# Kernel optimization log

Measured on AMD Instinct MI355X. Metric: run time of the kernel, lower is better.

## Reference

```python
import jax, jax.numpy as jnp
import numpy as np

N_WAY, N_SHOT, N_SEG = 3, 1, 4
SEGLEN, C, H, W = 16, 3, 112, 112
REG, COST_ALPHA, PHI = 7.0, 0.4, 1.0
SINK_ITERS = 100
# eval-mode BatchNorm with fresh stats (mean=0, var=1, gamma=1, beta=0) -> pure scale
BN_SCALE = np.float32(1.0 / np.sqrt(1.0 + 1e-5))

PARAM_NAMES = ['conv1_w', 'conv1_b', 'conv2_w', 'conv2_b', 'conv3a_w', 'conv3a_b',
               'conv3b_w', 'conv3b_b', 'conv4a_w', 'conv4a_b', 'conv4b_w', 'conv4b_b',
               'conv5a_w', 'conv5a_b', 'conv5b_w', 'conv5b_b', 'fc6_w', 'fc6_b',
               'fc7_w', 'fc7_b']


def _conv3d(x, w, b):
    y = jax.lax.conv_general_dilated(x, w, (1, 1, 1), [(1, 1)] * 3,
                                     dimension_numbers=('NCDHW', 'OIDHW', 'NCDHW'))
    return y + b[None, :, None, None, None]


def _maxpool(x, k, s, p=(0, 0, 0)):
    return jax.lax.reduce_window(x, -jnp.inf, jax.lax.max,
                                 (1, 1) + k, (1, 1) + s,
                                 [(0, 0), (0, 0)] + [(q, q) for q in p])


def _encode(x, p):
    r = jax.nn.relu
    x = r(BN_SCALE * _conv3d(x, p['conv1_w'], p['conv1_b']))
    x = _maxpool(x, (1, 2, 2), (1, 2, 2))
    x = r(BN_SCALE * _conv3d(x, p['conv2_w'], p['conv2_b']))
    x = _maxpool(x, (2, 2, 2), (2, 2, 2))
    x = r(_conv3d(x, p['conv3a_w'], p['conv3a_b']))
    x = r(BN_SCALE * _conv3d(x, p['conv3b_w'], p['conv3b_b']))
    x = _maxpool(x, (2, 2, 2), (2, 2, 2))
    x = r(_conv3d(x, p['conv4a_w'], p['conv4a_b']))
    x = r(BN_SCALE * _conv3d(x, p['conv4b_w'], p['conv4b_b']))
    x = _maxpool(x, (2, 2, 2), (2, 2, 2))
    x = r(_conv3d(x, p['conv5a_w'], p['conv5a_b']))
    x = r(BN_SCALE * _conv3d(x, p['conv5b_w'], p['conv5b_b']))
    x = _maxpool(x, (2, 2, 2), (2, 2, 2), (0, 1, 1))  # -> (N, 512, 1, 4, 4)
    x = x.reshape(-1, 8192)
    x = r(BN_SCALE * (x @ p['fc6_w'].T + p['fc6_b']))  # dropout identity in eval
    x = r(BN_SCALE * (x @ p['fc7_w'].T + p['fc7_b']))
    return x


def _positional_cost():
    t = jnp.arange(N_SEG, dtype=jnp.float32) / N_SEG
    d2 = (t[:, None] - t[None, :]) ** 2
    return jnp.exp(-(1.0 / PHI ** 2) * (1.0 / (d2 + 1.0)))


def _sinkhorn(cost):  # cost: (Q, S, n, n), uniform marginals 1/n
    n = cost.shape[-1]
    a = jnp.full((n,), 1.0 / n, cost.dtype)
    K = jnp.exp(-REG * cost)
    u0 = jnp.full(cost.shape[:-1], 1.0 / n, cost.dtype)

    def body(u, _):
        v = a / (jnp.einsum('qsij,qsi->qsj', K, u) + 1e-9)
        u = a / (jnp.einsum('qsij,qsj->qsi', K, v) + 1e-9)
        return u, None

    u, _ = jax.lax.scan(body, u0, None, length=SINK_ITERS)
    v = a / (jnp.einsum('qsij,qsi->qsj', K, u) + 1e-9)
    return u[..., :, None] * K * v[..., None, :]


def _forward(support_set, query_set, p):
    ts, tq = support_set.shape[0], query_set.shape[0]
    # (N, n_seg, seglen, c, h, w) -> (N*n_seg, c, seglen, h, w)
    sp = jnp.swapaxes(support_set, 2, 3).reshape(-1, C, SEGLEN, H, W)
    qr = jnp.swapaxes(query_set, 2, 3).reshape(-1, C, SEGLEN, H, W)
    sp = _encode(sp, p).reshape(ts, N_SEG, -1)
    qr = _encode(qr, p).reshape(tq, N_SEG, -1)
    qn = qr / (jnp.linalg.norm(qr, axis=-1, keepdims=True) + 1e-8)
    sn = sp / (jnp.linalg.norm(sp, axis=-1, keepdims=True) + 1e-8)
    sem_cost = 1.0 - jnp.einsum('qid,sjd->qsij', qn, sn)  # (Q, S, n_seg, n_seg)
    # positional cost only regularizes the OT solve; transport cost uses sem_cost
    solve_cost = sem_cost + COST_ALPHA * _positional_cost()
    plan = _sinkhorn(solve_cost)
    trans_cost = jnp.sum(plan * sem_cost, axis=(-2, -1))
    trans_cost = trans_cost.reshape(tq, N_WAY, N_SHOT).mean(-1)
    return -trans_cost


def setup_inputs() -> dict:
    key = jax.random.key(0)
    ks = iter(jax.random.split(key, 24))

    def cw(o, i):
        return jax.random.normal(next(ks), (o, i, 3, 3, 3), jnp.float32) * np.float32(np.sqrt(2.0 / (i * 27)))

    def fw(o, i):
        return jax.random.normal(next(ks), (o, i), jnp.float32) * np.float32(np.sqrt(2.0 / i))

    z = lambda n: jnp.zeros((n,), jnp.float32)
    return dict(
        support_set=jax.random.normal(next(ks), (N_WAY * N_SHOT, N_SEG, SEGLEN, C, H, W), jnp.float32),
        query_set=jax.random.normal(next(ks), (N_WAY, N_SEG, SEGLEN, C, H, W), jnp.float32),
        conv1_w=cw(64, 3), conv1_b=z(64),
        conv2_w=cw(128, 64), conv2_b=z(128),
        conv3a_w=cw(256, 128), conv3a_b=z(256),
        conv3b_w=cw(256, 256), conv3b_b=z(256),
        conv4a_w=cw(512, 256), conv4a_b=z(512),
        conv4b_w=cw(512, 512), conv4b_b=z(512),
        conv5a_w=cw(512, 512), conv5a_b=z(512),
        conv5b_w=cw(512, 512), conv5b_b=z(512),
        fc6_w=fw(4096, 8192), fc6_b=z(4096),
        fc7_w=fw(4096, 4096), fc7_b=z(4096),
    )


def reference(support_set, query_set, conv1_w, conv1_b, conv2_w, conv2_b,
              conv3a_w, conv3a_b, conv3b_w, conv3b_b, conv4a_w, conv4a_b,
              conv4b_w, conv4b_b, conv5a_w, conv5a_b, conv5b_w, conv5b_b,
              fc6_w, fc6_b, fc7_w, fc7_b):
    p = dict(zip(PARAM_NAMES, (conv1_w, conv1_b, conv2_w, conv2_b, conv3a_w, conv3a_b,
                               conv3b_w, conv3b_b, conv4a_w, conv4a_b, conv4b_w, conv4b_b,
                               conv5a_w, conv5a_b, conv5b_w, conv5b_b, fc6_w, fc6_b,
                               fc7_w, fc7_b)))
    return _forward(support_set, query_set, p)
```

## Files before the change

kernel.cpp:

```cpp
#include <hip/hip_runtime.h>
#include <hip/hip_bf16.h>
#include <cmath>

#define BN_SCALE_F 0.9999950000374997f

typedef __attribute__((ext_vector_type(8))) short short8;
typedef __attribute__((ext_vector_type(4))) float floatx4;

static __device__ __forceinline__ ushort f2bf(float x) {
    union { float f; unsigned u; } c; c.f = x;
    unsigned r = (c.u + 0x7FFFu + ((c.u >> 16) & 1u)) >> 16;
    return (ushort)r;
}
static __device__ __forceinline__ float bf2f(ushort h) {
    union { unsigned u; float f; } c; c.u = ((unsigned)h) << 16;
    return c.f;
}

__global__ __launch_bounds__(256) void repack_kernel(
    const float* __restrict__ w, ushort* __restrict__ oh, ushort* __restrict__ ol,
    int CI, int total)
{
    int idx = blockIdx.x * 256 + threadIdx.x;
    if (idx >= total) return;
    int ci = idx % CI;
    int t  = (idx / CI) % 27;
    int co = idx / (CI * 27);
    float v = w[((size_t)co * CI + ci) * 27 + t];
    ushort h = f2bf(v);
    oh[idx] = h;
    ol[idx] = f2bf(v - bf2f(h));
}

__global__ __launch_bounds__(256) void conv1_ndhwc(
    const float* __restrict__ sup, const float* __restrict__ qry, int clipBase,
    const float* __restrict__ wgt, const float* __restrict__ bias,
    ushort* __restrict__ outH, ushort* __restrict__ outL)
{
    __shared__ float sIn[4][10][12];
    __shared__ float sW[16][28];
    const int tid = threadIdx.x;
    const int bw = blockIdx.x % 14;
    const int bh = (blockIdx.x / 14) % 14;
    const int bd = blockIdx.x / 196;
    const int coL = tid >> 4;
    const int co  = blockIdx.y * 16 + coL;
    const int sp  = tid & 15;
    const int sh = sp >> 2, sw = sp & 3;
    const int n = blockIdx.z;
    const int clip = clipBase + n;
    const float* src = (clip < 12) ? (sup + (size_t)clip * 602112)
                                   : (qry + (size_t)(clip - 12) * 602112);
    const int d0 = 2 * bd, h0 = 8 * bh, w0 = 8 * bw;

    float acc[8] = {0.f,0.f,0.f,0.f,0.f,0.f,0.f,0.f};
    for (int ci = 0; ci < 3; ci++) {
        for (int t = tid; t < 832; t += 256) {
            if (t < 400) {
                int pd = t / 100; int rem = t - pd * 100;
                int ph = rem / 10; int pw = rem - ph * 10;
                int gd = d0 - 1 + pd, gh = h0 - 1 + ph, gw = w0 - 1 + pw;
                float v = 0.f;
                if ((unsigned)gd < 16u && (unsigned)gh < 112u && (unsigned)gw < 112u)
                    v = src[(size_t)gd * 37632 + ci * 12544 + gh * 112 + gw];
                sIn[pd][ph][pw] = v;
            } else {
                int t2 = t - 400;
                if (t2 < 432) {
                    int cl = t2 / 27, k = t2 - cl * 27;
                    sW[cl][k] = wgt[((size_t)(blockIdx.y * 16 + cl) * 3 + ci) * 27 + k];
                }
            }
        }
        __syncthreads();
        float wr[27];
#pragma unroll
        for (int k = 0; k < 27; k++) wr[k] = sW[coL][k];
#pragma unroll
        for (int dd = 0; dd < 4; dd++) {
            float qv[16];
#pragma unroll
            for (int hh = 0; hh < 4; hh++)
#pragma unroll
                for (int ww = 0; ww < 4; ww++)
                    qv[hh * 4 + ww] = sIn[dd][2 * sh + hh][2 * sw + ww];
#pragma unroll
            for (int kd = 0; kd < 3; kd++) {
                int deltad = dd - kd;
                if (deltad < 0 || deltad > 1) continue;
#pragma unroll
                for (int kh = 0; kh < 3; kh++)
#pragma unroll
                    for (int kw = 0; kw < 3; kw++) {
                        float wv = wr[kd * 9 + kh * 3 + kw];
#pragma unroll
                        for (int dh = 0; dh < 2; dh++)
#pragma unroll
                            for (int dw = 0; dw < 2; dw++)
                                acc[deltad * 4 + dh * 2 + dw] =
                                    fmaf(wv, qv[(dh + kh) * 4 + (dw + kw)],
                                         acc[deltad * 4 + dh * 2 + dw]);
                    }
            }
        }
        __syncthreads();
    }
    const float b = __ldg(bias + co);
    const int oh = 4 * bh + sh, ow = 4 * bw + sw;
#pragma unroll
    for (int dd = 0; dd < 2; dd++) {
        float m = 0.f;
#pragma unroll
        for (int k = 0; k < 4; k++) m = fmaxf(m, (acc[dd * 4 + k] + b) * BN_SCALE_F);
        size_t idx = ((((size_t)n * 16 + (d0 + dd)) * 56 + oh) * 56 + ow) * 64 + co;
        ushort h = f2bf(m);
        outH[idx] = h;
        outL[idx] = f2bf(m - bf2f(h));
    }
}

template<int CIN,int COUT,int D,int H,int W,int MODE>
__global__ __launch_bounds__(256,1) void conv_mfma(
    const ushort* __restrict__ inH, const ushort* __restrict__ inL,
    const ushort* __restrict__ wH,  const ushort* __restrict__ wL,
    const float* __restrict__ bias,
    ushort* __restrict__ outH, ushort* __restrict__ outL, float* __restrict__ outF)
{
    constexpr int TW = (W + 7) / 8;
    constexpr int TH = (H + 7) / 8;
    __shared__ ushort sMem[19200 * 2 + 6144 * 2];
    ushort* sPH = sMem;
    ushort* sPL = sMem + 19200;
    ushort* sWH = sMem + 38400;
    ushort* sWL = sMem + 44544;

    const int tid = threadIdx.x;
    const int lane = tid & 63;
    const int wv = tid >> 6;
    const int n15 = lane & 15;
    const int g4 = lane >> 4;
    const int tw = blockIdx.x % TW;
    const int th = (blockIdx.x / TW) % TH;
    const int td = blockIdx.x / (TW * TH);
    const int coG0 = blockIdx.y * 64;
    const int n = blockIdx.z;

    int sdv[4], shv[4], swv[4];
#pragma unroll
    for (int spg = 0; spg < 4; spg++) {
        int s = wv * 64 + spg * 16 + n15;
        sdv[spg] = s >> 6; shv[spg] = (s >> 3) & 7; swv[spg] = s & 7;
    }

    const size_t inBase = (size_t)n * CIN * D * H * W;

    floatx4 acc[4][4];
#pragma unroll
    for (int i = 0; i < 4; i++)
#pragma unroll
        for (int j = 0; j < 4; j++) acc[i][j] = (floatx4){0.f, 0.f, 0.f, 0.f};

    uint4 pfH[3], pfL[3];

    for (int c0 = 0; c0 < CIN; c0 += 32) {
        for (int t = tid; t < 2400; t += 256) {
            int pos = t >> 2, g = t & 3;
            int pd = pos / 100; int rem = pos - pd * 100;
            int ph = rem / 10;  int pw = rem - ph * 10;
            int gd = td * 4 - 1 + pd;
            int gh = th * 8 - 1 + ph;
            int gw = tw * 8 - 1 + pw;
            uint4 vh = {0u,0u,0u,0u}, vl = {0u,0u,0u,0u};
            if ((unsigned)gd < (unsigned)D && (unsigned)gh < (unsigned)H && (unsigned)gw < (unsigned)W) {
                size_t gi = inBase + (((size_t)gd * H + gh) * W + gw) * CIN + c0 + g * 8;
                vh = *(const uint4*)(inH + gi);
                vl = *(const uint4*)(inL + gi);
            }
            *(uint4*)(sPH + pos * 32 + g * 8) = vh;
            *(uint4*)(sPL + pos * 32 + g * 8) = vl;
        }
        if (c0 == 0) {
#pragma unroll
            for (int k = 0; k < 3; k++) {
                int t = tid + k * 256;
                int kw = t >> 8, col = (t >> 2) & 63, g8 = t & 3;
                size_t src = ((size_t)(coG0 + col) * 27 + kw) * CIN + g8 * 8;
                pfH[k] = *(const uint4*)(wH + src);
                pfL[k] = *(const uint4*)(wL + src);
            }
        }
        __syncthreads();

        for (int row = 0; row < 9; row++) {
#pragma unroll
            for (int k = 0; k < 3; k++) {
                int t = tid + k * 256;
                int kw = t >> 8, col = (t >> 2) & 63, g8 = t & 3;
                int dst = (kw * 64 + col) * 32 + g8 * 8;
                *(uint4*)(sWH + dst) = pfH[k];
                *(uint4*)(sWL + dst) = pfL[k];
            }
            __syncthreads();
            {
                int nc0 = c0, nrow = row + 1;
                if (nrow == 9) { nrow = 0; nc0 = c0 + 32; }
                if (nc0 < CIN) {
#pragma unroll
                    for (int k = 0; k < 3; k++) {
                        int t = tid + k * 256;
                        int kw = t >> 8, col = (t >> 2) & 63, g8 = t & 3;
                        size_t src = ((size_t)(coG0 + col) * 27 + nrow * 3 + kw) * CIN + nc0 + g8 * 8;
                        pfH[k] = *(const uint4*)(wH + src);
                        pfL[k] = *(const uint4*)(wL + src);
                    }
                }
            }
            const int kd = row / 3, kh = row - kd * 3;
            int pbase[4];
#pragma unroll
            for (int spg = 0; spg < 4; spg++)
                pbase[spg] = ((sdv[spg] + kd) * 10 + shv[spg] + kh) * 10 + swv[spg];
#pragma unroll
            for (int kw = 0; kw < 3; kw++) {
                short8 Bh[4], Bl[4];
#pragma unroll
                for (int spg = 0; spg < 4; spg++) {
                    int off = (pbase[spg] + kw) * 32 + g4 * 8;
                    Bh[spg] = *(const short8*)(sPH + off);
                    Bl[spg] = *(const short8*)(sPL + off);
                }
#pragma unroll
                for (int cog = 0; cog < 4; cog++) {
                    int offA = (kw * 64 + cog * 16 + n15) * 32 + g4 * 8;
                    short8 Ah = *(const short8*)(sWH + offA);
                    short8 Al = *(const short8*)(sWL + offA);
#pragma unroll
                    for (int spg = 0; spg < 4; spg++) {
                        acc[cog][spg] = __builtin_amdgcn_mfma_f32_16x16x32_bf16(Ah, Bh[spg], acc[cog][spg], 0, 0, 0);
                        acc[cog][spg] = __builtin_amdgcn_mfma_f32_16x16x32_bf16(Ah, Bl[spg], acc[cog][spg], 0, 0, 0);
                        acc[cog][spg] = __builtin_amdgcn_mfma_f32_16x16x32_bf16(Al, Bh[spg], acc[cog][spg], 0, 0, 0);
                    }
                }
            }
            __syncthreads();
        }
    }

    float* sEp = (float*)sMem;
#pragma unroll
    for (int cog = 0; cog < 4; cog++)
#pragma unroll
        for (int spg = 0; spg < 4; spg++) {
            int sp = wv * 64 + spg * 16 + n15;
#pragma unroll
            for (int r = 0; r < 4; r++) {
                int co = cog * 16 + g4 * 4 + r;
                sEp[sp * 65 + co] = acc[cog][spg][r];
            }
        }
    __syncthreads();

    const int co = tid & 63;
    const int coG = coG0 + co;
    const float b = __ldg(bias + coG);

    if constexpr (MODE == 0) {
#pragma unroll 4
        for (int i = 0; i < 64; i++) {
            int sp = i * 4 + (tid >> 6);
            int ld = sp >> 6, lh = (sp >> 3) & 7, lw = sp & 7;
            int gd = td * 4 + ld, gh = th * 8 + lh, gw = tw * 8 + lw;
            if (gh < H && gw < W) {
                float y = fmaxf(sEp[sp * 65 + co] + b, 0.f);
                size_t idx = ((((size_t)n * D + gd) * H + gh) * W + gw) * COUT + coG;
                ushort h = f2bf(y);
                outH[idx] = h;
                outL[idx] = f2bf(y - bf2f(h));
            }
        }
    } else {
        constexpr int OD = D / 2, OH = H / 2, OW = W / 2;
#pragma unroll
        for (int i = 0; i < 8; i++) {
            int pp = i * 4 + (tid >> 6);
            int ppd = pp >> 4, pph = (pp >> 2) & 3, ppw = pp & 3;
            int gpd = td * 2 + ppd, gph = th * 4 + pph, gpw = tw * 4 + ppw;
            if (gph < OH && gpw < OW) {
                float m = -1e30f;
#pragma unroll
                for (int dd = 0; dd < 2; dd++)
#pragma unroll
                    for (int dh = 0; dh < 2; dh++)
#pragma unroll
                        for (int dw = 0; dw < 2; dw++) {
                            int sp = (ppd * 2 + dd) * 64 + (pph * 2 + dh) * 8 + (ppw * 2 + dw);
                            m = fmaxf(m, sEp[sp * 65 + co]);
                        }
                float y = fmaxf((m + b) * BN_SCALE_F, 0.f);
                if constexpr (MODE == 1) {
                    size_t idx = ((((size_t)n * OD + gpd) * OH + gph) * OW + gpw) * COUT + coG;
                    ushort h = f2bf(y);
                    outH[idx] = h;
                    outL[idx] = f2bf(y - bf2f(h));
                } else {
                    size_t idx = ((((size_t)n * COUT + coG) * OD + gpd) * OH + gph) * OW + gpw;
                    outF[idx] = y;
                }
            }
        }
    }
}

template<int CIN,int COUT,int D,int H,int W,int MODE>
__global__ __launch_bounds__(256) void conv_tile(
    const float* __restrict__ in,
    const float* __restrict__ wgt, const float* __restrict__ bias,
    float* __restrict__ out)
{
    constexpr int PAD = (MODE == 3) ? 1 : 0;
    constexpr int OD  = (MODE == 0) ? D : D / 2;
    constexpr int OH  = (MODE == 0) ? H : (H + 2 * PAD) / 2;
    constexpr int OW  = (MODE == 0) ? W : (W + 2 * PAD) / 2;
    constexpr int TH  = (MODE == 0) ? (H + 7) / 8 : (OH + 3) / 4;
    constexpr int TW  = (MODE == 0) ? (W + 7) / 8 : (OW + 3) / 4;
    constexpr int HW  = H * W;
    constexpr int CC  = 2;

    __shared__ float sIn[CC][4][10][12];
    __shared__ float sW[CC][16][28];

    const int tid = threadIdx.x;
    const int bw = blockIdx.x % TW;
    const int bh = (blockIdx.x / TW) % TH;
    const int bd = blockIdx.x / (TW * TH);
    const int coL = tid >> 4;
    const int co  = blockIdx.y * 16 + coL;
    const int sp  = tid & 15;
    const int sh = sp >> 2, sw = sp & 3;
    const int n = blockIdx.z;

    const int d0 = 2 * bd, h0 = 8 * bh - PAD, w0 = 8 * bw - PAD;
    const int ht = h0 + 2 * sh, wt = w0 + 2 * sw;

    const float* src = in + (size_t)n * CIN * D * HW;

    float acc[8] = {0.f,0.f,0.f,0.f,0.f,0.f,0.f,0.f};

    for (int ci0 = 0; ci0 < CIN; ci0 += CC) {
        for (int t = tid; t < CC * 400 + CC * 432; t += 256) {
            if (t < CC * 400) {
                int c = t / 400, r = t % 400;
                int pd = r / 100, ph = (r / 10) % 10, pw = r % 10;
                int gd = d0 - 1 + pd, gh = h0 - 1 + ph, gw = w0 - 1 + pw;
                float v = 0.f;
                if (gd >= 0 && gd < D && gh >= 0 && gh < H && gw >= 0 && gw < W)
                    v = src[(size_t)(ci0 + c) * D * HW + gd * HW + gh * W + gw];
                sIn[c][pd][ph][pw] = v;
            } else {
                int t2 = t - CC * 400;
                int c = t2 / 432, r = t2 % 432;
                int cl = r / 27, k = r % 27;
                sW[c][cl][k] = wgt[((size_t)(blockIdx.y * 16 + cl) * CIN + (ci0 + c)) * 27 + k];
            }
        }
        __syncthreads();
        for (int c = 0; c < CC; c++) {
            float wr[27];
#pragma unroll
            for (int k = 0; k < 27; k++) wr[k] = sW[c][coL][k];
#pragma unroll
            for (int dd = 0; dd < 4; dd++) {
                float qv[16];
#pragma unroll
                for (int hh = 0; hh < 4; hh++)
#pragma unroll
                    for (int ww = 0; ww < 4; ww++)
                        qv[hh * 4 + ww] = sIn[c][dd][2 * sh + hh][2 * sw + ww];
#pragma unroll
                for (int kd = 0; kd < 3; kd++) {
                    int deltad = dd - kd;
                    if (deltad < 0 || deltad > 1) continue;
#pragma unroll
                    for (int kh = 0; kh < 3; kh++)
#pragma unroll
                        for (int kw = 0; kw < 3; kw++) {
                            float wv = wr[kd * 9 + kh * 3 + kw];
#pragma unroll
                            for (int dh = 0; dh < 2; dh++)
#pragma unroll
                                for (int dw = 0; dw < 2; dw++)
                                    acc[deltad * 4 + dh * 2 + dw] =
                                        fmaf(wv, qv[(dh + kh) * 4 + (dw + kw)],
                                             acc[deltad * 4 + dh * 2 + dw]);
                        }
                }
            }
        }
        __syncthreads();
    }

    const float b = __ldg(bias + co);
    if constexpr (MODE == 0) {
#pragma unroll
        for (int dd = 0; dd < 2; dd++) {
            int d = d0 + dd; if (d >= D) continue;
#pragma unroll
            for (int dh = 0; dh < 2; dh++) {
                int h = ht + dh; if (h < 0 || h >= H) continue;
#pragma unroll
                for (int dw = 0; dw < 2; dw++) {
                    int w = wt + dw; if (w < 0 || w >= W) continue;
                    out[(((size_t)n * COUT + co) * D + d) * HW + h * W + w] =
                        fmaxf(acc[dd * 4 + dh * 2 + dw] + b, 0.f);
                }
            }
        }
    } else {
        int oh = 4 * bh + sh, ow = 4 * bw + sw;
        if (oh < OH && ow < OW) {
            float m = 0.f;
#pragma unroll
            for (int dd2 = 0; dd2 < 2; dd2++)
#pragma unroll
                for (int dh = 0; dh < 2; dh++) {
                    int h = ht + dh; if (PAD && (h < 0 || h >= H)) continue;
#pragma unroll
                    for (int dw = 0; dw < 2; dw++) {
                        int w = wt + dw; if (PAD && (w < 0 || w >= W)) continue;
                        m = fmaxf(m, (acc[dd2 * 4 + dh * 2 + dw] + b) * BN_SCALE_F);
                    }
                }
            out[(((size_t)n * COUT + co) * OD + bd) * (OH * OW) + oh * OW + ow] = m;
        }
    }
}

__global__ __launch_bounds__(256) void fc_kernel(
    const float* __restrict__ x, const float* __restrict__ wgt,
    const float* __restrict__ bias, float* __restrict__ out,
    int K, int Cout, int total)
{
    int gt = blockIdx.x * 256 + threadIdx.x;
    int wid = gt >> 6;
    int lane = gt & 63;
    if (wid >= total) return;
    int co = wid % Cout; int n = wid / Cout;
    const float4* xp = (const float4*)(x + (size_t)n * K);
    const float4* wp = (const float4*)(wgt + (size_t)co * K);
    int K4 = K >> 2;
    float s = 0.f;
    for (int k = lane; k < K4; k += 64) {
        float4 a = __ldg(xp + k), b = __ldg(wp + k);
        s += a.x * b.x + a.y * b.y + a.z * b.z + a.w * b.w;
    }
#pragma unroll
    for (int off = 32; off > 0; off >>= 1) s += __shfl_down(s, off, 64);
    if (lane == 0) {
        float y = (s + __ldg(bias + co)) * BN_SCALE_F;
        out[wid] = fmaxf(y, 0.f);
    }
}

__global__ __launch_bounds__(256) void dots_kernel(
    const float* __restrict__ feat, float* __restrict__ dots)
{
    int task = blockIdx.x; int tid = threadIdx.x;
    int ra, rb;
    if (task < 24) { ra = task; rb = task; }
    else {
        int t = task - 24;
        int q = t / 48; int r = t % 48;
        int i = r / 12; int s = (r % 12) / 4; int j = r % 4;
        ra = 12 + q * 4 + i;
        rb = s * 4 + j;
    }
    const float4* A = (const float4*)(feat + (size_t)ra * 4096);
    const float4* B = (const float4*)(feat + (size_t)rb * 4096);
    float acc = 0.f;
    for (int k = tid; k < 1024; k += 256) {
        float4 a = A[k], b = B[k];
        acc += a.x * b.x + a.y * b.y + a.z * b.z + a.w * b.w;
    }
#pragma unroll
    for (int off = 32; off > 0; off >>= 1) acc += __shfl_down(acc, off, 64);
    __shared__ float red[4];
    if ((tid & 63) == 0) red[tid >> 6] = acc;
    __syncthreads();
    if (tid == 0) dots[task] = red[0] + red[1] + red[2] + red[3];
}

__global__ __launch_bounds__(64) void sinkhorn_kernel(
    const float* __restrict__ dots, float* __restrict__ out)
{
    int t = threadIdx.x;
    if (t >= 9) return;
    int q = t / 3, s = t % 3;
    float Km[16], sem[16];
#pragma unroll
    for (int i = 0; i < 4; i++) {
        float nq = sqrtf(dots[12 + q * 4 + i]) + 1e-8f;
#pragma unroll
        for (int j = 0; j < 4; j++) {
            float ns = sqrtf(dots[s * 4 + j]) + 1e-8f;
            float d = dots[24 + q * 48 + i * 12 + s * 4 + j];
            float c = 1.0f - d / (nq * ns);
            float ti = i * 0.25f, tj = j * 0.25f;
            float d2 = (ti - tj) * (ti - tj);
            float pc = expf(-1.0f / (d2 + 1.0f));
            sem[i * 4 + j] = c;
            Km[i * 4 + j] = expf(-7.0f * (c + 0.4f * pc));
        }
    }
    float u[4] = {0.25f, 0.25f, 0.25f, 0.25f}, v[4];
    for (int it = 0; it < 100; it++) {
#pragma unroll
        for (int j = 0; j < 4; j++) {
            float sj = Km[j] * u[0] + Km[4 + j] * u[1] + Km[8 + j] * u[2] + Km[12 + j] * u[3];
            v[j] = 0.25f / (sj + 1e-9f);
        }
#pragma unroll
        for (int i = 0; i < 4; i++) {
            float si = Km[i * 4] * v[0] + Km[i * 4 + 1] * v[1] + Km[i * 4 + 2] * v[2] + Km[i * 4 + 3] * v[3];
            u[i] = 0.25f / (si + 1e-9f);
        }
    }
#pragma unroll
    for (int j = 0; j < 4; j++) {
        float sj = Km[j] * u[0] + Km[4 + j] * u[1] + Km[8 + j] * u[2] + Km[12 + j] * u[3];
        v[j] = 0.25f / (sj + 1e-9f);
    }
    float tc = 0.f;
#pragma unroll
    for (int i = 0; i < 4; i++)
#pragma unroll
        for (int j = 0; j < 4; j++)
            tc += u[i] * Km[i * 4 + j] * v[j] * sem[i * 4 + j];
    out[q * 3 + s] = -tc;
}

extern "C" void kernel_launch(void* const* d_in, const int* in_sizes, int n_in,
                              void* d_out, int out_size, void* d_ws, size_t ws_size,
                              hipStream_t stream)
{
    const float* sup = (const float*)d_in[0];
    const float* qry = (const float*)d_in[1];
    const float* w1  = (const float*)d_in[2];  const float* b1  = (const float*)d_in[3];
    const float* w2  = (const float*)d_in[4];  const float* b2  = (const float*)d_in[5];
    const float* w3a = (const float*)d_in[6];  const float* b3a = (const float*)d_in[7];
    const float* w3b = (const float*)d_in[8];  const float* b3b = (const float*)d_in[9];
    const float* w4a = (const float*)d_in[10]; const float* b4a = (const float*)d_in[11];
    const float* w4b = (const float*)d_in[12]; const float* b4b = (const float*)d_in[13];
    const float* w5a = (const float*)d_in[14]; const float* b5a = (const float*)d_in[15];
    const float* w5b = (const float*)d_in[16]; const float* b5b = (const float*)d_in[17];
    const float* w6  = (const float*)d_in[18]; const float* b6  = (const float*)d_in[19];
    const float* w7  = (const float*)d_in[20]; const float* b7  = (const float*)d_in[21];
    float* out = (float*)d_out;

    char* wsB = (char*)d_ws;
    size_t off = 0;
    auto carve = [&](size_t bytes) -> char* {
        char* p = wsB + off;
        off = (off + bytes + 255) & ~(size_t)255;
        return p;
    };

    const int RW2 = 128 * 27 * 64, RW3a = 256 * 27 * 128, RW3b = 256 * 27 * 256;
    const int RW4a = 512 * 27 * 256, RW4b = 512 * 27 * 512;
    ushort* w2H  = (ushort*)carve((size_t)RW2 * 2);  ushort* w2L  = (ushort*)carve((size_t)RW2 * 2);
    ushort* w3aH = (ushort*)carve((size_t)RW3a * 2); ushort* w3aL = (ushort*)carve((size_t)RW3a * 2);
    ushort* w3bH = (ushort*)carve((size_t)RW3b * 2); ushort* w3bL = (ushort*)carve((size_t)RW3b * 2);
    ushort* w4aH = (ushort*)carve((size_t)RW4a * 2); ushort* w4aL = (ushort*)carve((size_t)RW4a * 2);
    ushort* w4bH = (ushort*)carve((size_t)RW4b * 2); ushort* w4bL = (ushort*)carve((size_t)RW4b * 2);

    float* x4b24 = (float*)carve((size_t)24 * 50176 * 4);
    float* x5a24 = (float*)carve((size_t)24 * 50176 * 4);
    float* x5b24 = (float*)carve((size_t)24 * 8192 * 4);
    float* fc6o  = (float*)carve((size_t)24 * 4096 * 4);
    float* feat  = (float*)carve((size_t)24 * 4096 * 4);
    float* dotsb = (float*)carve(256 * 4);

    const size_t fixed = off;
    const long long P1 = 3211264LL, P2 = 802816LL;
    const long long perG = (P1 + P2) * 2 * 2;
    int G = 1;
    const int cands[8] = {24, 12, 8, 6, 4, 3, 2, 1};
    for (int k = 0; k < 8; k++) {
        if (fixed + (size_t)(perG * cands[k]) + 4096 <= ws_size) { G = cands[k]; break; }
    }
    ushort* AH = (ushort*)carve((size_t)G * P1 * 2);
    ushort* AL = (ushort*)carve((size_t)G * P1 * 2);
    ushort* BH = (ushort*)carve((size_t)G * P2 * 2);
    ushort* BL = (ushort*)carve((size_t)G * P2 * 2);

    repack_kernel<<<(RW2  + 255) / 256, 256, 0, stream>>>(w2,  w2H,  w2L,  64,  RW2);
    repack_kernel<<<(RW3a + 255) / 256, 256, 0, stream>>>(w3a, w3aH, w3aL, 128, RW3a);
    repack_kernel<<<(RW3b + 255) / 256, 256, 0, stream>>>(w3b, w3bH, w3bL, 256, RW3b);
    repack_kernel<<<(RW4a + 255) / 256, 256, 0, stream>>>(w4a, w4aH, w4aL, 256, RW4a);
    repack_kernel<<<(RW4b + 255) / 256, 256, 0, stream>>>(w4b, w4bH, w4bL, 512, RW4b);

    for (int base = 0; base < 24; base += G) {
        conv1_ndhwc<<<dim3(1568, 4, G), 256, 0, stream>>>(sup, qry, base, w1, b1, AH, AL);
        conv_mfma<64, 128, 16, 56, 56, 1><<<dim3(196, 2, G), 256, 0, stream>>>(
            AH, AL, w2H, w2L, b2, BH, BL, nullptr);
        conv_mfma<128, 256, 8, 28, 28, 0><<<dim3(32, 4, G), 256, 0, stream>>>(
            BH, BL, w3aH, w3aL, b3a, AH, AL, nullptr);
        conv_mfma<256, 256, 8, 28, 28, 1><<<dim3(32, 4, G), 256, 0, stream>>>(
            AH, AL, w3bH, w3bL, b3b, BH, BL, nullptr);
        conv_mfma<256, 512, 4, 14, 14, 0><<<dim3(4, 8, G), 256, 0, stream>>>(
            BH, BL, w4aH, w4aL, b4a, AH, AL, nullptr);
        conv_mfma<512, 512, 4, 14, 14, 2><<<dim3(4, 8, G), 256, 0, stream>>>(
            AH, AL, w4bH, w4bL, b4b, nullptr, nullptr, x4b24 + (size_t)base * 50176);
    }

    conv_tile<512, 512, 2, 7, 7, 0><<<dim3(1, 32, 24), 256, 0, stream>>>(x4b24, w5a, b5a, x5a24);
    conv_tile<512, 512, 2, 7, 7, 3><<<dim3(1, 32, 24), 256, 0, stream>>>(x5a24, w5b, b5b, x5b24);
    int t6 = 24 * 4096;
    fc_kernel<<<(t6 * 64 + 255) / 256, 256, 0, stream>>>(x5b24, w6, b6, fc6o, 8192, 4096, t6);
    fc_kernel<<<(t6 * 64 + 255) / 256, 256, 0, stream>>>(fc6o, w7, b7, feat, 4096, 4096, t6);
    dots_kernel<<<168, 256, 0, stream>>>(feat, dotsb);
    sinkhorn_kernel<<<1, 64, 0, stream>>>(dotsb, out);
}
```

Measured before the change: 10.78 ms.

## Move conv5 to MFMA path, swizzle LDS, batch FC over samples

Conv5a and conv5b now run on the split-bf16 MFMA conv kernel, with a new epilogue mode that fuses the padded max-pool and writes the flattened features. The scalar fp32 conv_tile kernel is removed. LDS tiles for inputs and weights get an XOR swizzle to reduce bank conflicts. The FC kernel now computes all 24 samples per weight row, so each weight is read once instead of 24 times, at the cost of 24 accumulators per lane and more registers.

```diff
diff --git a/kernel.cpp b/kernel.cpp
--- a/kernel.cpp
+++ b/kernel.cpp
@@ -176,8 +176,9 @@
                 vh = *(const uint4*)(inH + gi);
                 vl = *(const uint4*)(inL + gi);
             }
-            *(uint4*)(sPH + pos * 32 + g * 8) = vh;
-            *(uint4*)(sPL + pos * 32 + g * 8) = vl;
+            int sg = g ^ ((pos >> 1) & 3);
+            *(uint4*)(sPH + pos * 32 + sg * 8) = vh;
+            *(uint4*)(sPL + pos * 32 + sg * 8) = vl;
         }
         if (c0 == 0) {
 #pragma unroll
@@ -196,7 +197,8 @@
             for (int k = 0; k < 3; k++) {
                 int t = tid + k * 256;
                 int kw = t >> 8, col = (t >> 2) & 63, g8 = t & 3;
-                int dst = (kw * 64 + col) * 32 + g8 * 8;
+                int wpos = kw * 64 + col;
+                int dst = wpos * 32 + (g8 ^ ((wpos >> 1) & 3)) * 8;
                 *(uint4*)(sWH + dst) = pfH[k];
                 *(uint4*)(sWL + dst) = pfL[k];
             }
@@ -225,13 +227,15 @@
                 short8 Bh[4], Bl[4];
 #pragma unroll
                 for (int spg = 0; spg < 4; spg++) {
-                    int off = (pbase[spg] + kw) * 32 + g4 * 8;
+                    int p = pbase[spg] + kw;
+                    int off = p * 32 + (g4 ^ ((p >> 1) & 3)) * 8;
                     Bh[spg] = *(const short8*)(sPH + off);
                     Bl[spg] = *(const short8*)(sPL + off);
                 }
 #pragma unroll
                 for (int cog = 0; cog < 4; cog++) {
-                    int offA = (kw * 64 + cog * 16 + n15) * 32 + g4 * 8;
+                    int pa = kw * 64 + cog * 16 + n15;
+                    int offA = pa * 32 + (g4 ^ ((pa >> 1) & 3)) * 8;
                     short8 Ah = *(const short8*)(sWH + offA);
                     short8 Al = *(const short8*)(sWL + offA);
 #pragma unroll
@@ -270,13 +274,34 @@
             int sp = i * 4 + (tid >> 6);
             int ld = sp >> 6, lh = (sp >> 3) & 7, lw = sp & 7;
             int gd = td * 4 + ld, gh = th * 8 + lh, gw = tw * 8 + lw;
-            if (gh < H && gw < W) {
+            if (gd < D && gh < H && gw < W) {
                 float y = fmaxf(sEp[sp * 65 + co] + b, 0.f);
                 size_t idx = ((((size_t)n * D + gd) * H + gh) * W + gw) * COUT + coG;
                 ushort h = f2bf(y);
                 outH[idx] = h;
                 outL[idx] = f2bf(y - bf2f(h));
             }
+        }
+    } else if constexpr (MODE == 3) {
+#pragma unroll
+        for (int i = 0; i < 4; i++) {
+            int pp = i * 4 + (tid >> 6);
+            int oh = pp >> 2, ow = pp & 3;
+            float m = -1e30f;
+#pragma unroll
+            for (int dd = 0; dd < 2; dd++)
+#pragma unroll
+                for (int dh = 0; dh < 2; dh++) {
+                    int h = 2 * oh - 1 + dh; if (h < 0 || h >= 7) continue;
+#pragma unroll
+                    for (int dw = 0; dw < 2; dw++) {
+                        int w = 2 * ow - 1 + dw; if (w < 0 || w >= 7) continue;
+                        int sp = dd * 64 + h * 8 + w;
+                        m = fmaxf(m, sEp[sp * 65 + co]);
+                    }
+                }
+            float y = fmaxf((m + b) * BN_SCALE_F, 0.f);
+            outF[(size_t)n * 8192 + (size_t)coG * 16 + oh * 4 + ow] = y;
         }
     } else {
         constexpr int OD = D / 2, OH = H / 2, OW = W / 2;
@@ -311,153 +336,35 @@
     }
 }
 
-template<int CIN,int COUT,int D,int H,int W,int MODE>
-__global__ __launch_bounds__(256) void conv_tile(
-    const float* __restrict__ in,
-    const float* __restrict__ wgt, const float* __restrict__ bias,
-    float* __restrict__ out)
-{
-    constexpr int PAD = (MODE == 3) ? 1 : 0;
-    constexpr int OD  = (MODE == 0) ? D : D / 2;
-    constexpr int OH  = (MODE == 0) ? H : (H + 2 * PAD) / 2;
-    constexpr int OW  = (MODE == 0) ? W : (W + 2 * PAD) / 2;
-    constexpr int TH  = (MODE == 0) ? (H + 7) / 8 : (OH + 3) / 4;
-    constexpr int TW  = (MODE == 0) ? (W + 7) / 8 : (OW + 3) / 4;
-    constexpr int HW  = H * W;
-    constexpr int CC  = 2;
-
-    __shared__ float sIn[CC][4][10][12];
-    __shared__ float sW[CC][16][28];
-
-    const int tid = threadIdx.x;
-    const int bw = blockIdx.x % TW;
-    const int bh = (blockIdx.x / TW) % TH;
-    const int bd = blockIdx.x / (TW * TH);
-    const int coL = tid >> 4;
-    const int co  = blockIdx.y * 16 + coL;
-    const int sp  = tid & 15;
-    const int sh = sp >> 2, sw = sp & 3;
-    const int n = blockIdx.z;
-
-    const int d0 = 2 * bd, h0 = 8 * bh - PAD, w0 = 8 * bw - PAD;
-    const int ht = h0 + 2 * sh, wt = w0 + 2 * sw;
-
-    const float* src = in + (size_t)n * CIN * D * HW;
-
-    float acc[8] = {0.f,0.f,0.f,0.f,0.f,0.f,0.f,0.f};
-
-    for (int ci0 = 0; ci0 < CIN; ci0 += CC) {
-        for (int t = tid; t < CC * 400 + CC * 432; t += 256) {
-            if (t < CC * 400) {
-                int c = t / 400, r = t % 400;
-                int pd = r / 100, ph = (r / 10) % 10, pw = r % 10;
-                int gd = d0 - 1 + pd, gh = h0 - 1 + ph, gw = w0 - 1 + pw;
-                float v = 0.f;
-                if (gd >= 0 && gd < D && gh >= 0 && gh < H && gw >= 0 && gw < W)
-                    v = src[(size_t)(ci0 + c) * D * HW + gd * HW + gh * W + gw];
-                sIn[c][pd][ph][pw] = v;
-            } else {
-                int t2 = t - CC * 400;
-                int c = t2 / 432, r = t2 % 432;
-                int cl = r / 27, k = r % 27;
-                sW[c][cl][k] = wgt[((size_t)(blockIdx.y * 16 + cl) * CIN + (ci0 + c)) * 27 + k];
-            }
-        }
-        __syncthreads();
-        for (int c = 0; c < CC; c++) {
-            float wr[27];
-#pragma unroll
-            for (int k = 0; k < 27; k++) wr[k] = sW[c][coL][k];
-#pragma unroll
-            for (int dd = 0; dd < 4; dd++) {
-                float qv[16];
-#pragma unroll
-                for (int hh = 0; hh < 4; hh++)
-#pragma unroll
-                    for (int ww = 0; ww < 4; ww++)
-                        qv[hh * 4 + ww] = sIn[c][dd][2 * sh + hh][2 * sw + ww];
-#pragma unroll
-                for (int kd = 0; kd < 3; kd++) {
-                    int deltad = dd - kd;
-                    if (deltad < 0 || deltad > 1) continue;
-#pragma unroll
-                    for (int kh = 0; kh < 3; kh++)
-#pragma unroll
-                        for (int kw = 0; kw < 3; kw++) {
-                            float wv = wr[kd * 9 + kh * 3 + kw];
-#pragma unroll
-                            for (int dh = 0; dh < 2; dh++)
-#pragma unroll
-                                for (int dw = 0; dw < 2; dw++)
-                                    acc[deltad * 4 + dh * 2 + dw] =
-                                        fmaf(wv, qv[(dh + kh) * 4 + (dw + kw)],
-                                             acc[deltad * 4 + dh * 2 + dw]);
-                        }
-                }
-            }
-        }
-        __syncthreads();
-    }
-
-    const float b = __ldg(bias + co);
-    if constexpr (MODE == 0) {
-#pragma unroll
-        for (int dd = 0; dd < 2; dd++) {
-            int d = d0 + dd; if (d >= D) continue;
-#pragma unroll
-            for (int dh = 0; dh < 2; dh++) {
-                int h = ht + dh; if (h < 0 || h >= H) continue;
-#pragma unroll
-                for (int dw = 0; dw < 2; dw++) {
-                    int w = wt + dw; if (w < 0 || w >= W) continue;
-                    out[(((size_t)n * COUT + co) * D + d) * HW + h * W + w] =
-                        fmaxf(acc[dd * 4 + dh * 2 + dw] + b, 0.f);
-                }
-            }
-        }
-    } else {
-        int oh = 4 * bh + sh, ow = 4 * bw + sw;
-        if (oh < OH && ow < OW) {
-            float m = 0.f;
-#pragma unroll
-            for (int dd2 = 0; dd2 < 2; dd2++)
-#pragma unroll
-                for (int dh = 0; dh < 2; dh++) {
-                    int h = ht + dh; if (PAD && (h < 0 || h >= H)) continue;
-#pragma unroll
-                    for (int dw = 0; dw < 2; dw++) {
-                        int w = wt + dw; if (PAD && (w < 0 || w >= W)) continue;
-                        m = fmaxf(m, (acc[dd2 * 4 + dh * 2 + dw] + b) * BN_SCALE_F);
-                    }
-                }
-            out[(((size_t)n * COUT + co) * OD + bd) * (OH * OW) + oh * OW + ow] = m;
-        }
-    }
-}
-
 __global__ __launch_bounds__(256) void fc_kernel(
     const float* __restrict__ x, const float* __restrict__ wgt,
     const float* __restrict__ bias, float* __restrict__ out,
-    int K, int Cout, int total)
-{
-    int gt = blockIdx.x * 256 + threadIdx.x;
-    int wid = gt >> 6;
-    int lane = gt & 63;
-    if (wid >= total) return;
-    int co = wid % Cout; int n = wid / Cout;
-    const float4* xp = (const float4*)(x + (size_t)n * K);
+    int K, int Cout)
+{
+    int co = (blockIdx.x * 256 + threadIdx.x) >> 6;
+    int lane = threadIdx.x & 63;
+    if (co >= Cout) return;
     const float4* wp = (const float4*)(wgt + (size_t)co * K);
     int K4 = K >> 2;
-    float s = 0.f;
+    float s[24];
+#pragma unroll
+    for (int n = 0; n < 24; n++) s[n] = 0.f;
     for (int k = lane; k < K4; k += 64) {
-        float4 a = __ldg(xp + k), b = __ldg(wp + k);
-        s += a.x * b.x + a.y * b.y + a.z * b.z + a.w * b.w;
-    }
-#pragma unroll
-    for (int off = 32; off > 0; off >>= 1) s += __shfl_down(s, off, 64);
-    if (lane == 0) {
-        float y = (s + __ldg(bias + co)) * BN_SCALE_F;
-        out[wid] = fmaxf(y, 0.f);
+        float4 b = __ldg(wp + k);
+#pragma unroll
+        for (int n = 0; n < 24; n++) {
+            float4 a = __ldg((const float4*)(x + (size_t)n * K) + k);
+            s[n] += a.x * b.x + a.y * b.y + a.z * b.z + a.w * b.w;
+        }
+    }
+    const float bb = __ldg(bias + co);
+#pragma unroll
+    for (int n = 0; n < 24; n++) {
+        float v = s[n];
+#pragma unroll
+        for (int off = 32; off > 0; off >>= 1) v += __shfl_down(v, off, 64);
+        if (lane == 0)
+            out[(size_t)n * Cout + co] = fmaxf((v + bb) * BN_SCALE_F, 0.f);
     }
 }
 
@@ -565,15 +472,19 @@
     };
 
     const int RW2 = 128 * 27 * 64, RW3a = 256 * 27 * 128, RW3b = 256 * 27 * 256;
-    const int RW4a = 512 * 27 * 256, RW4b = 512 * 27 * 512;
+    const int RW4a = 512 * 27 * 256, RW4b = 512 * 27 * 512, RW5 = 512 * 27 * 512;
     ushort* w2H  = (ushort*)carve((size_t)RW2 * 2);  ushort* w2L  = (ushort*)carve((size_t)RW2 * 2);
     ushort* w3aH = (ushort*)carve((size_t)RW3a * 2); ushort* w3aL = (ushort*)carve((size_t)RW3a * 2);
     ushort* w3bH = (ushort*)carve((size_t)RW3b * 2); ushort* w3bL = (ushort*)carve((size_t)RW3b * 2);
     ushort* w4aH = (ushort*)carve((size_t)RW4a * 2); ushort* w4aL = (ushort*)carve((size_t)RW4a * 2);
     ushort* w4bH = (ushort*)carve((size_t)RW4b * 2); ushort* w4bL = (ushort*)carve((size_t)RW4b * 2);
-
-    float* x4b24 = (float*)carve((size_t)24 * 50176 * 4);
-    float* x5a24 = (float*)carve((size_t)24 * 50176 * 4);
+    ushort* w5aH = (ushort*)carve((size_t)RW5 * 2);  ushort* w5aL = (ushort*)carve((size_t)RW5 * 2);
+    ushort* w5bH = (ushort*)carve((size_t)RW5 * 2);  ushort* w5bL = (ushort*)carve((size_t)RW5 * 2);
+
+    ushort* c4H = (ushort*)carve((size_t)24 * 50176 * 2);
+    ushort* c4L = (ushort*)carve((size_t)24 * 50176 * 2);
+    ushort* c5H = (ushort*)carve((size_t)24 * 50176 * 2);
+    ushort* c5L = (ushort*)carve((size_t)24 * 50176 * 2);
     float* x5b24 = (float*)carve((size_t)24 * 8192 * 4);
     float* fc6o  = (float*)carve((size_t)24 * 4096 * 4);
     float* feat  = (float*)carve((size_t)24 * 4096 * 4);
@@ -597,6 +508,8 @@
     repack_kernel<<<(RW3b + 255) / 256, 256, 0, stream>>>(w3b, w3bH, w3bL, 256, RW3b);
     repack_kernel<<<(RW4a + 255) / 256, 256, 0, stream>>>(w4a, w4aH, w4aL, 256, RW4a);
     repack_kernel<<<(RW4b + 255) / 256, 256, 0, stream>>>(w4b, w4bH, w4bL, 512, RW4b);
+    repack_kernel<<<(RW5  + 255) / 256, 256, 0, stream>>>(w5a, w5aH, w5aL, 512, RW5);
+    repack_kernel<<<(RW5  + 255) / 256, 256, 0, stream>>>(w5b, w5bH, w5bL, 512, RW5);
 
     for (int base = 0; base < 24; base += G) {
         conv1_ndhwc<<<dim3(1568, 4, G), 256, 0, stream>>>(sup, qry, base, w1, b1, AH, AL);
@@ -608,15 +521,18 @@
             AH, AL, w3bH, w3bL, b3b, BH, BL, nullptr);
         conv_mfma<256, 512, 4, 14, 14, 0><<<dim3(4, 8, G), 256, 0, stream>>>(
             BH, BL, w4aH, w4aL, b4a, AH, AL, nullptr);
-        conv_mfma<512, 512, 4, 14, 14, 2><<<dim3(4, 8, G), 256, 0, stream>>>(
-            AH, AL, w4bH, w4bL, b4b, nullptr, nullptr, x4b24 + (size_t)base * 50176);
-    }
-
-    conv_tile<512, 512, 2, 7, 7, 0><<<dim3(1, 32, 24), 256, 0, stream>>>(x4b24, w5a, b5a, x5a24);
-    conv_tile<512, 512, 2, 7, 7, 3><<<dim3(1, 32, 24), 256, 0, stream>>>(x5a24, w5b, b5b, x5b24);
-    int t6 = 24 * 4096;
-    fc_kernel<<<(t6 * 64 + 255) / 256, 256, 0, stream>>>(x5b24, w6, b6, fc6o, 8192, 4096, t6);
-    fc_kernel<<<(t6 * 64 + 255) / 256, 256, 0, stream>>>(fc6o, w7, b7, feat, 4096, 4096, t6);
+        conv_mfma<512, 512, 4, 14, 14, 1><<<dim3(4, 8, G), 256, 0, stream>>>(
+            AH, AL, w4bH, w4bL, b4b,
+            c4H + (size_t)base * 50176, c4L + (size_t)base * 50176, nullptr);
+    }
+
+    conv_mfma<512, 512, 2, 7, 7, 0><<<dim3(1, 8, 24), 256, 0, stream>>>(
+        c4H, c4L, w5aH, w5aL, b5a, c5H, c5L, nullptr);
+    conv_mfma<512, 512, 2, 7, 7, 3><<<dim3(1, 8, 24), 256, 0, stream>>>(
+        c5H, c5L, w5bH, w5bL, b5b, nullptr, nullptr, x5b24);
+
+    fc_kernel<<<(4096 * 64 + 255) / 256, 256, 0, stream>>>(x5b24, w6, b6, fc6o, 8192, 4096);
+    fc_kernel<<<(4096 * 64 + 255) / 256, 256, 0, stream>>>(fc6o, w7, b7, feat, 4096, 4096);
     dots_kernel<<<168, 256, 0, stream>>>(feat, dotsb);
     sinkhorn_kernel<<<1, 64, 0, stream>>>(dotsb, out);
 }
```

Measured after the change: 9.332 ms. -13.5%, faster.
